# Kernel optimization log

Hardware: AMD Instinct MI355X
Metric: run time of the kernel (lower is better)

## Reference

```python
import jax, jax.numpy as jnp
import numpy as np

NUM_GRAPHS = 8
EV_A3_TO_GPA = 160.21766208


def _energy(pos, bond_vec, src, dst, edge_graph, centers, W1, b1, W2, b2, W3, b3):
    # Surrogate GNN energy: edge displacement mixes pos and bond_vec so both get grads,
    # mirroring grad(total_energies, [pos, bond_vec]) in the original wrapper.
    disp = bond_vec + pos[dst] - pos[src]                      # [E,3]
    d = jnp.sqrt(jnp.sum(disp * disp, axis=-1) + 1e-12)        # [E]
    rbf = jnp.exp(-jnp.square(d[:, None] - centers[None, :]))  # [E,K]
    h = jax.nn.silu(rbf @ W1 + b1)                             # [E,H]
    h = jax.nn.silu(h @ W2 + b2)                               # [E,H]
    e_edge = (h @ W3 + b3)[:, 0]                               # [E]
    return jax.ops.segment_sum(e_edge, edge_graph, num_segments=NUM_GRAPHS)  # [B]


def setup_inputs() -> dict:
    key = jax.random.key(0)
    ks = jax.random.split(key, 8)
    N, E, K, H = 49152, 786432, 32, 64
    pos = jax.random.normal(ks[0], (N, 3), jnp.float32) * 3.0
    bond_vec = jax.random.normal(ks[1], (E, 3), jnp.float32)
    src = jax.random.randint(ks[2], (E,), 0, N, dtype=jnp.int32)
    dst = jax.random.randint(ks[3], (E,), 0, N, dtype=jnp.int32)
    edge_graph = jnp.repeat(jnp.arange(NUM_GRAPHS, dtype=jnp.int32), E // NUM_GRAPHS)
    volume = jax.random.uniform(ks[4], (N,), jnp.float32, 50.0, 150.0)
    centers = jnp.linspace(0.0, 5.0, K).astype(jnp.float32)
    W1 = jax.random.normal(ks[5], (K, H), jnp.float32) / np.float32(np.sqrt(K))
    b1 = jnp.zeros((H,), jnp.float32)
    W2 = jax.random.normal(ks[6], (H, H), jnp.float32) / np.float32(np.sqrt(H))
    b2 = jnp.zeros((H,), jnp.float32)
    W3 = jax.random.normal(ks[7], (H, 1), jnp.float32) / np.float32(np.sqrt(H))
    b3 = jnp.zeros((1,), jnp.float32)
    return {"pos": pos, "bond_vec": bond_vec, "src": src, "dst": dst,
            "edge_graph": edge_graph, "volume": volume, "centers": centers,
            "W1": W1, "b1": b1, "W2": W2, "b2": b2, "W3": W3, "b3": b3}


def reference(pos, bond_vec, src, dst, edge_graph, volume, centers, W1, b1, W2, b2, W3, b3):
    energies, vjp_fn = jax.vjp(
        lambda p, bv: _energy(p, bv, src, dst, edge_graph, centers, W1, b1, W2, b2, W3, b3),
        pos, bond_vec)
    # grad_outputs = ones_like(total_energies)
    gpos, gbv = vjp_fn(jnp.ones_like(energies))
    forces = -gpos                                             # [N,3]
    f_ij = -gbv                                                # [E,3]
    # Per-graph stress: bond_vec_g^T @ f_ij_g, vectorized as segment-summed outer products.
    outer = bond_vec[:, :, None] * f_ij[:, None, :]            # [E,3,3]
    S = jax.ops.segment_sum(outer, edge_graph, num_segments=NUM_GRAPHS)  # [B,3,3]
    nodes_per_graph = pos.shape[0] // NUM_GRAPHS
    vol0 = volume[jnp.arange(NUM_GRAPHS) * nodes_per_graph]    # volume at first node of each graph
    stresses = (-EV_A3_TO_GPA * S / vol0[:, None, None]).reshape(NUM_GRAPHS * 3, 3)
    hessian = jnp.zeros((1,), jnp.float32)                     # calc_hessian=False
    return energies, forces, stresses, hessian
```

## Files before the change

### kernel.cpp

```cpp
#include <hip/hip_runtime.h>
#include <math.h>

#define K_RBF 32
#define H_DIM 64
#define TBL 4096
#define D_MAX 16.0f
#define N_NODES 49152
#define N_EDGES 786432
#define N_GRAPHS 8
#define NODES_PER_GRAPH 6144
#define EV_A3_TO_GPA 160.21766208f
#define LOG2E 1.44269504088896f

#define OUT_FORCES 8
#define OUT_STRESS 147464
#define OUT_TAIL_N 81

#define CHUNK_NODES  192
#define CHUNK_FLOATS 576
#define N_CHUNKS     256
#define REC_CAP      7168

#define EDGE_BLOCKS   384
#define EDGE_THREADS  1024
#define EDGES_PER_GRAPH (N_EDGES / N_GRAPHS)
#define BLK_PER_GRAPH 48

#define OFF_TAB 0u
#define OFF_CNT 32768u
#define OFF_REC 33792u
#define WS_NEED (OFF_REC + (size_t)N_CHUNKS * REC_CAP * 16u)

__device__ __forceinline__ int chunk_of(int node) {
    return (int)((unsigned)((node >> 6) * 683) >> 11);
}

__global__ __launch_bounds__(256) void build_table(
    const float* __restrict__ centers,
    const float* __restrict__ W1, const float* __restrict__ b1,
    const float* __restrict__ W2, const float* __restrict__ b2,
    const float* __restrict__ W3, const float* __restrict__ b3,
    float2* __restrict__ tab, int* __restrict__ gcnt,
    float* __restrict__ out, int zero_out_tail)
{
    if (blockIdx.x == 0) {
        int t = threadIdx.x;
        gcnt[t] = 0;
        if (zero_out_tail) {
            if (t < N_GRAPHS) out[t] = 0.f;
            else if (t < OUT_TAIL_N) out[3 * N_NODES + t] = 0.f;
        }
    }

    __shared__ float W2s[H_DIM * 65];
    for (int idx = threadIdx.x; idx < H_DIM * H_DIM; idx += 256)
        W2s[(idx >> 6) * 65 + (idx & 63)] = W2[idx];
    __syncthreads();

    int lane = threadIdx.x & 63;
    int i    = blockIdx.x * 4 + (threadIdx.x >> 6);
    float d  = (float)i * (D_MAX / (float)TBL);

    float z1 = b1[lane], u = 0.f;
#pragma unroll
    for (int k = 0; k < K_RBF; ++k) {
        float tc = d - centers[k];
        float e  = exp2f(-tc * tc * LOG2E);
        float w  = W1[k * H_DIM + lane];
        z1 = fmaf(e, w, z1);
        u  = fmaf(-2.f * tc * e, w, u);
    }
    float s1  = 1.f / (1.f + exp2f(-z1 * LOG2E));
    float h1  = z1 * s1;
    float ds1 = s1 * fmaf(z1, 1.f - s1, 1.f);

    float z2 = b2[lane];
#pragma unroll
    for (int h = 0; h < H_DIM; ++h)
        z2 = fmaf(__shfl(h1, h, 64), W2s[h * 65 + lane], z2);

    float s2  = 1.f / (1.f + exp2f(-z2 * LOG2E));
    float w3  = W3[lane];
    float Fp  = z2 * s2 * w3;
    float dz2 = w3 * s2 * fmaf(z2, 1.f - s2, 1.f);

    float dh1 = 0.f;
#pragma unroll
    for (int j = 0; j < H_DIM; ++j)
        dh1 = fmaf(__shfl(dz2, j, 64), W2s[lane * 65 + j], dh1);

    float Gp = dh1 * ds1 * u;
#pragma unroll
    for (int m = 32; m > 0; m >>= 1) {
        Fp += __shfl_xor(Fp, m, 64);
        Gp += __shfl_xor(Gp, m, 64);
    }
    if (lane == 0) tab[i] = make_float2(Fp + b3[0], Gp);
}

__global__ __launch_bounds__(EDGE_THREADS) void edge_compute(
    const float* __restrict__ pos, const float* __restrict__ bond,
    const int* __restrict__ src, const int* __restrict__ dst,
    const float* __restrict__ volume, const float2* __restrict__ tab,
    float4* __restrict__ recs, int* __restrict__ gcnt,
    float* __restrict__ out)
{
    __shared__ int   cnt[N_CHUNKS];
    __shared__ int   basech[N_CHUNKS];
    __shared__ float red[16][10];

    const int t = threadIdx.x;
    if (t < N_CHUNKS) cnt[t] = 0;
    __syncthreads();

    const int g = blockIdx.x & 7;
    const int w = blockIdx.x >> 3;
    const int base_e = g * EDGES_PER_GRAPH + w * (EDGE_THREADS * 2);

    float vacc[10];
#pragma unroll
    for (int q = 0; q < 10; ++q) vacc[q] = 0.f;

    int   edi[2], esi[2], es0[2], es1[2];
    float egx[2], egy[2], egz[2];

#pragma unroll
    for (int i = 0; i < 2; ++i) {
        int e  = base_e + i * EDGE_THREADS + t;
        int si = src[e], di = dst[e];
        float bx = bond[3 * e + 0], by = bond[3 * e + 1], bz = bond[3 * e + 2];
        float dx = bx + pos[3 * di + 0] - pos[3 * si + 0];
        float dy = by + pos[3 * di + 1] - pos[3 * si + 1];
        float dz = bz + pos[3 * di + 2] - pos[3 * si + 2];
        float d  = sqrtf(fmaf(dx, dx, fmaf(dy, dy, fmaf(dz, dz, 1e-12f))));

        float tt  = fminf(d * ((float)TBL / D_MAX), (float)(TBL - 1));
        int   ix  = min((int)tt, TBL - 2);
        float fr  = tt - (float)ix;
        float2 ta = tab[ix], tb2 = tab[ix + 1];
        float F = fmaf(fr, tb2.x - ta.x, ta.x);
        float G = fmaf(fr, tb2.y - ta.y, ta.y);

        float scl = G / d;
        float gx = scl * dx, gy = scl * dy, gz = scl * dz;
        egx[i] = gx; egy[i] = gy; egz[i] = gz;
        edi[i] = di; esi[i] = si;
        es0[i] = atomicAdd(&cnt[chunk_of(di)], 1);
        es1[i] = atomicAdd(&cnt[chunk_of(si)], 1);

        vacc[0] += F;
        vacc[1] = fmaf(bx, gx, vacc[1]); vacc[2] = fmaf(bx, gy, vacc[2]);
        vacc[3] = fmaf(bx, gz, vacc[3]); vacc[4] = fmaf(by, gx, vacc[4]);
        vacc[5] = fmaf(by, gy, vacc[5]); vacc[6] = fmaf(by, gz, vacc[6]);
        vacc[7] = fmaf(bz, gx, vacc[7]); vacc[8] = fmaf(bz, gy, vacc[8]);
        vacc[9] = fmaf(bz, gz, vacc[9]);
    }
    __syncthreads();
    if (t < N_CHUNKS) basech[t] = atomicAdd(&gcnt[t], cnt[t]);
    __syncthreads();
#pragma unroll
    for (int i = 0; i < 2; ++i) {
        int c0 = chunk_of(edi[i]), c1 = chunk_of(esi[i]);
        int l0 = edi[i] - c0 * CHUNK_NODES;
        int l1 = esi[i] - c1 * CHUNK_NODES;
        int p0 = basech[c0] + es0[i];
        int p1 = basech[c1] + es1[i];
        if (p0 < REC_CAP)
            recs[(size_t)c0 * REC_CAP + p0] =
                make_float4(-egx[i], -egy[i], -egz[i], __int_as_float(l0));
        if (p1 < REC_CAP)
            recs[(size_t)c1 * REC_CAP + p1] =
                make_float4(egx[i], egy[i], egz[i], __int_as_float(l1));
    }

#pragma unroll
    for (int q = 0; q < 10; ++q) {
        float x = vacc[q];
#pragma unroll
        for (int m = 32; m > 0; m >>= 1) x += __shfl_xor(x, m, 64);
        vacc[q] = x;
    }
    int wave = t >> 6;
    if ((t & 63) == 0)
#pragma unroll
        for (int q = 0; q < 10; ++q) red[wave][q] = vacc[q];
    __syncthreads();
    if (t < 10) {
        float tot = 0.f;
#pragma unroll
        for (int k = 0; k < 16; ++k) tot += red[k][t];
        if (t == 0) atomicAdd(out + g, tot);
        else {
            float vol = volume[g * NODES_PER_GRAPH];
            atomicAdd(out + OUT_STRESS + g * 9 + (t - 1),
                      tot * (EV_A3_TO_GPA / vol));
        }
    }
}

__global__ __launch_bounds__(512) void scatter_direct(
    const float4* __restrict__ recs, const int* __restrict__ gcnt,
    float* __restrict__ out)
{
    __shared__ float acc[CHUNK_FLOATS];
    const int t = threadIdx.x;
    if (t < CHUNK_FLOATS) acc[t] = 0.f;
    if (t < CHUNK_FLOATS - 512) acc[512 + t] = 0.f;
    __syncthreads();

    const int c = blockIdx.x;
    int total = min(gcnt[c], REC_CAP);
    const float4* seg = recs + (size_t)c * REC_CAP;
    for (int r = t; r < total; r += 512) {
        float4 rec = seg[r];
        int li = 3 * __float_as_int(rec.w);
        atomicAdd(&acc[li + 0], rec.x);
        atomicAdd(&acc[li + 1], rec.y);
        atomicAdd(&acc[li + 2], rec.z);
    }
    __syncthreads();

    if (t < CHUNK_FLOATS / 4) {
        float4* dst4 = (float4*)(out + OUT_FORCES + c * CHUNK_FLOATS);
        dst4[t] = ((const float4*)acc)[t];
    }
}

__global__ __launch_bounds__(256) void edge_fallback(
    const float* __restrict__ pos, const float* __restrict__ bond,
    const int* __restrict__ src, const int* __restrict__ dst,
    const float* __restrict__ volume, const float2* __restrict__ tab,
    float* __restrict__ out)
{
    __shared__ float red[4][10];
    int lb = (blockIdx.x & 7) * (EDGES_PER_GRAPH / 256) + (blockIdx.x >> 3);
    int g  = blockIdx.x & 7;
    int e  = lb * 256 + threadIdx.x;

    int si = src[e], di = dst[e];
    float bx = bond[3 * e + 0], by = bond[3 * e + 1], bz = bond[3 * e + 2];
    float dx = bx + pos[3 * di + 0] - pos[3 * si + 0];
    float dy = by + pos[3 * di + 1] - pos[3 * si + 1];
    float dz = bz + pos[3 * di + 2] - pos[3 * si + 2];
    float d  = sqrtf(fmaf(dx, dx, fmaf(dy, dy, fmaf(dz, dz, 1e-12f))));

    float tt  = fminf(d * ((float)TBL / D_MAX), (float)(TBL - 1));
    int   ix  = min((int)tt, TBL - 2);
    float fr  = tt - (float)ix;
    float2 ta = tab[ix], tb2 = tab[ix + 1];
    float F = fmaf(fr, tb2.x - ta.x, ta.x);
    float G = fmaf(fr, tb2.y - ta.y, ta.y);
    float scl = G / d;
    float gx = scl * dx, gy = scl * dy, gz = scl * dz;

    float* forces = out + OUT_FORCES;
    atomicAdd(forces + 3 * di + 0, -gx);
    atomicAdd(forces + 3 * di + 1, -gy);
    atomicAdd(forces + 3 * di + 2, -gz);
    atomicAdd(forces + 3 * si + 0,  gx);
    atomicAdd(forces + 3 * si + 1,  gy);
    atomicAdd(forces + 3 * si + 2,  gz);

    float v[10] = { F,
                    bx * gx, bx * gy, bx * gz,
                    by * gx, by * gy, by * gz,
                    bz * gx, bz * gy, bz * gz };
#pragma unroll
    for (int q = 0; q < 10; ++q) {
        float x = v[q];
#pragma unroll
        for (int m = 32; m > 0; m >>= 1) x += __shfl_xor(x, m, 64);
        v[q] = x;
    }
    int wave = threadIdx.x >> 6;
    if ((threadIdx.x & 63) == 0)
#pragma unroll
        for (int q = 0; q < 10; ++q) red[wave][q] = v[q];
    __syncthreads();
    if (threadIdx.x < 10) {
        float tot = red[0][threadIdx.x] + red[1][threadIdx.x]
                  + red[2][threadIdx.x] + red[3][threadIdx.x];
        if (threadIdx.x == 0) atomicAdd(out + g, tot);
        else {
            float vol = volume[g * NODES_PER_GRAPH];
            atomicAdd(out + OUT_STRESS + g * 9 + (threadIdx.x - 1),
                      tot * (EV_A3_TO_GPA / vol));
        }
    }
}

extern "C" void kernel_launch(void* const* d_in, const int* in_sizes, int n_in,
                              void* d_out, int out_size, void* d_ws, size_t ws_size,
                              hipStream_t stream)
{
    const float* pos     = (const float*)d_in[0];
    const float* bond    = (const float*)d_in[1];
    const int*   src     = (const int*)d_in[2];
    const int*   dst     = (const int*)d_in[3];
    const float* volume  = (const float*)d_in[5];
    const float* centers = (const float*)d_in[6];
    const float* W1 = (const float*)d_in[7];
    const float* b1 = (const float*)d_in[8];
    const float* W2 = (const float*)d_in[9];
    const float* b2 = (const float*)d_in[10];
    const float* W3 = (const float*)d_in[11];
    const float* b3 = (const float*)d_in[12];
    float*  out  = (float*)d_out;
    char*   ws   = (char*)d_ws;
    float2* tab  = (float2*)(ws + OFF_TAB);
    int*    gcnt = (int*)(ws + OFF_CNT);
    float4* recs = (float4*)(ws + OFF_REC);

    if (ws_size >= WS_NEED) {
        build_table<<<TBL / 4, 256, 0, stream>>>(centers, W1, b1, W2, b2, W3, b3,
                                                 tab, gcnt, out, 1);
        edge_compute<<<EDGE_BLOCKS, EDGE_THREADS, 0, stream>>>(
            pos, bond, src, dst, volume, tab, recs, gcnt, out);
        scatter_direct<<<N_CHUNKS, 512, 0, stream>>>(recs, gcnt, out);
    } else {
        hipMemsetAsync(d_out, 0, (size_t)out_size * sizeof(float), stream);
        build_table<<<TBL / 4, 256, 0, stream>>>(centers, W1, b1, W2, b2, W3, b3,
                                                 tab, gcnt, out, 0);
        edge_fallback<<<N_EDGES / 256, 256, 0, stream>>>(
            pos, bond, src, dst, volume, tab, out);
    }
}
```

Measured before the change: 150.7 us.

## Fuse table build, edge compute and scatter into one persistent kernel

After: 196.5 us. +30.4%, slower.

```diff
diff --git a/kernel.cpp b/kernel.cpp
--- a/kernel.cpp
+++ b/kernel.cpp
@@ -21,46 +21,30 @@
 #define N_CHUNKS     256
 #define REC_CAP      7168
 
-#define EDGE_BLOCKS   384
-#define EDGE_THREADS  1024
+#define FUSED_BLOCKS  256
+#define FUSED_THREADS 1024
+#define EDGES_PER_BLOCK 3072
 #define EDGES_PER_GRAPH (N_EDGES / N_GRAPHS)
-#define BLK_PER_GRAPH 48
-
-#define OFF_TAB 0u
-#define OFF_CNT 32768u
-#define OFF_REC 33792u
+#define BLK_PER_GRAPH 32
+#define TBL_PER_BLOCK 16
+
+#define OFF_TAB  0u
+#define OFF_CNT  32768u
+#define OFF_DONE 33792u
+#define OFF_REC  34816u
 #define WS_NEED (OFF_REC + (size_t)N_CHUNKS * REC_CAP * 16u)
 
 __device__ __forceinline__ int chunk_of(int node) {
     return (int)((unsigned)((node >> 6) * 683) >> 11);
 }
 
-__global__ __launch_bounds__(256) void build_table(
-    const float* __restrict__ centers,
+__device__ __forceinline__ float2 mlp_entry(
+    int i, int lane, const float* __restrict__ centers,
     const float* __restrict__ W1, const float* __restrict__ b1,
-    const float* __restrict__ W2, const float* __restrict__ b2,
-    const float* __restrict__ W3, const float* __restrict__ b3,
-    float2* __restrict__ tab, int* __restrict__ gcnt,
-    float* __restrict__ out, int zero_out_tail)
-{
-    if (blockIdx.x == 0) {
-        int t = threadIdx.x;
-        gcnt[t] = 0;
-        if (zero_out_tail) {
-            if (t < N_GRAPHS) out[t] = 0.f;
-            else if (t < OUT_TAIL_N) out[3 * N_NODES + t] = 0.f;
-        }
-    }
-
-    __shared__ float W2s[H_DIM * 65];
-    for (int idx = threadIdx.x; idx < H_DIM * H_DIM; idx += 256)
-        W2s[(idx >> 6) * 65 + (idx & 63)] = W2[idx];
-    __syncthreads();
-
-    int lane = threadIdx.x & 63;
-    int i    = blockIdx.x * 4 + (threadIdx.x >> 6);
+    const float* __restrict__ W2s, const float* __restrict__ b2,
+    const float* __restrict__ W3, const float* __restrict__ b3)
+{
     float d  = (float)i * (D_MAX / (float)TBL);
-
     float z1 = b1[lane], u = 0.f;
 #pragma unroll
     for (int k = 0; k < K_RBF; ++k) {
@@ -95,38 +79,72 @@
         Fp += __shfl_xor(Fp, m, 64);
         Gp += __shfl_xor(Gp, m, 64);
     }
-    if (lane == 0) tab[i] = make_float2(Fp + b3[0], Gp);
-}
-
-__global__ __launch_bounds__(EDGE_THREADS) void edge_compute(
+    return make_float2(Fp + b3[0], Gp);
+}
+
+__global__ __launch_bounds__(FUSED_THREADS, 4) void fused_all(
     const float* __restrict__ pos, const float* __restrict__ bond,
     const int* __restrict__ src, const int* __restrict__ dst,
-    const float* __restrict__ volume, const float2* __restrict__ tab,
-    float4* __restrict__ recs, int* __restrict__ gcnt,
-    float* __restrict__ out)
-{
-    __shared__ int   cnt[N_CHUNKS];
+    const float* __restrict__ volume, const float* __restrict__ centers,
+    const float* __restrict__ W1, const float* __restrict__ b1,
+    const float* __restrict__ W2, const float* __restrict__ b2,
+    const float* __restrict__ W3, const float* __restrict__ b3,
+    float2* __restrict__ tab, int* __restrict__ gcnt, int* __restrict__ done,
+    float4* __restrict__ recs, float* __restrict__ out)
+{
+    __shared__ float W2s[H_DIM * 65];
+    __shared__ int   cntl[N_CHUNKS];
     __shared__ int   basech[N_CHUNKS];
     __shared__ float red[16][10];
+    __shared__ float acc[4 * 577];
 
     const int t = threadIdx.x;
-    if (t < N_CHUNKS) cnt[t] = 0;
-    __syncthreads();
-
-    const int g = blockIdx.x & 7;
-    const int w = blockIdx.x >> 3;
-    const int base_e = g * EDGES_PER_GRAPH + w * (EDGE_THREADS * 2);
+    const int b = blockIdx.x;
+    const int lane = t & 63, wv = t >> 6;
+
+    for (int idx = t; idx < H_DIM * H_DIM; idx += FUSED_THREADS)
+        W2s[(idx >> 6) * 65 + (idx & 63)] = W2[idx];
+    if (b == 0) {
+        if (t < N_CHUNKS) gcnt[t] = 0;
+        if (t == 512) done[1] = 0;
+        if (t < N_GRAPHS) out[t] = 0.f;
+        else if (t >= 8 && t < OUT_TAIL_N) out[OUT_STRESS + t - 8] = 0.f;
+    }
+    __syncthreads();
+
+    {
+        int i = b * TBL_PER_BLOCK + wv;
+        float2 fg = mlp_entry(i, lane, centers, W1, b1, W2s, b2, W3, b3);
+        if (lane == 0) tab[i] = fg;
+    }
+    __syncthreads();
+
+    if (t == 0) {
+        __hip_atomic_fetch_add(&done[0], 1, __ATOMIC_RELEASE,
+                               __HIP_MEMORY_SCOPE_AGENT);
+        while (__hip_atomic_load(&done[0], __ATOMIC_ACQUIRE,
+                                 __HIP_MEMORY_SCOPE_AGENT) < FUSED_BLOCKS)
+            __builtin_amdgcn_s_sleep(2);
+    }
+    __syncthreads();
+
+    if (t < N_CHUNKS) cntl[t] = 0;
+    __syncthreads();
+
+    const int g = b >> 5;
+    const int w = b & 31;
+    const int base_e = g * EDGES_PER_GRAPH + w * EDGES_PER_BLOCK;
 
     float vacc[10];
 #pragma unroll
     for (int q = 0; q < 10; ++q) vacc[q] = 0.f;
 
-    int   edi[2], esi[2], es0[2], es1[2];
-    float egx[2], egy[2], egz[2];
-
-#pragma unroll
-    for (int i = 0; i < 2; ++i) {
-        int e  = base_e + i * EDGE_THREADS + t;
+    int   edi[3], esi[3], es0[3], es1[3];
+    float egx[3], egy[3], egz[3];
+
+#pragma unroll
+    for (int i = 0; i < 3; ++i) {
+        int e  = base_e + i * FUSED_THREADS + t;
         int si = src[e], di = dst[e];
         float bx = bond[3 * e + 0], by = bond[3 * e + 1], bz = bond[3 * e + 2];
         float dx = bx + pos[3 * di + 0] - pos[3 * si + 0];
@@ -145,8 +163,8 @@
         float gx = scl * dx, gy = scl * dy, gz = scl * dz;
         egx[i] = gx; egy[i] = gy; egz[i] = gz;
         edi[i] = di; esi[i] = si;
-        es0[i] = atomicAdd(&cnt[chunk_of(di)], 1);
-        es1[i] = atomicAdd(&cnt[chunk_of(si)], 1);
+        es0[i] = atomicAdd(&cntl[chunk_of(di)], 1);
+        es1[i] = atomicAdd(&cntl[chunk_of(si)], 1);
 
         vacc[0] += F;
         vacc[1] = fmaf(bx, gx, vacc[1]); vacc[2] = fmaf(bx, gy, vacc[2]);
@@ -156,10 +174,11 @@
         vacc[9] = fmaf(bz, gz, vacc[9]);
     }
     __syncthreads();
-    if (t < N_CHUNKS) basech[t] = atomicAdd(&gcnt[t], cnt[t]);
-    __syncthreads();
-#pragma unroll
-    for (int i = 0; i < 2; ++i) {
+    if (t < N_CHUNKS) basech[t] = atomicAdd(&gcnt[t], cntl[t]);
+    __syncthreads();
+
+#pragma unroll
+    for (int i = 0; i < 3; ++i) {
         int c0 = chunk_of(edi[i]), c1 = chunk_of(esi[i]);
         int l0 = edi[i] - c0 * CHUNK_NODES;
         int l1 = esi[i] - c1 * CHUNK_NODES;
@@ -180,10 +199,9 @@
         for (int m = 32; m > 0; m >>= 1) x += __shfl_xor(x, m, 64);
         vacc[q] = x;
     }
-    int wave = t >> 6;
-    if ((t & 63) == 0)
-#pragma unroll
-        for (int q = 0; q < 10; ++q) red[wave][q] = vacc[q];
+    if (lane == 0)
+#pragma unroll
+        for (int q = 0; q < 10; ++q) red[wv][q] = vacc[q];
     __syncthreads();
     if (t < 10) {
         float tot = 0.f;
@@ -196,34 +214,56 @@
                       tot * (EV_A3_TO_GPA / vol));
         }
     }
-}
-
-__global__ __launch_bounds__(512) void scatter_direct(
-    const float4* __restrict__ recs, const int* __restrict__ gcnt,
-    float* __restrict__ out)
-{
-    __shared__ float acc[CHUNK_FLOATS];
-    const int t = threadIdx.x;
-    if (t < CHUNK_FLOATS) acc[t] = 0.f;
-    if (t < CHUNK_FLOATS - 512) acc[512 + t] = 0.f;
-    __syncthreads();
-
-    const int c = blockIdx.x;
-    int total = min(gcnt[c], REC_CAP);
-    const float4* seg = recs + (size_t)c * REC_CAP;
-    for (int r = t; r < total; r += 512) {
-        float4 rec = seg[r];
-        int li = 3 * __float_as_int(rec.w);
-        atomicAdd(&acc[li + 0], rec.x);
-        atomicAdd(&acc[li + 1], rec.y);
-        atomicAdd(&acc[li + 2], rec.z);
-    }
-    __syncthreads();
-
-    if (t < CHUNK_FLOATS / 4) {
-        float4* dst4 = (float4*)(out + OUT_FORCES + c * CHUNK_FLOATS);
-        dst4[t] = ((const float4*)acc)[t];
-    }
+    __syncthreads();
+
+    if (t == 0) {
+        __hip_atomic_fetch_add(&done[1], 1, __ATOMIC_RELEASE,
+                               __HIP_MEMORY_SCOPE_AGENT);
+        while (__hip_atomic_load(&done[1], __ATOMIC_ACQUIRE,
+                                 __HIP_MEMORY_SCOPE_AGENT) < FUSED_BLOCKS)
+            __builtin_amdgcn_s_sleep(2);
+    }
+    __syncthreads();
+
+    for (int j = t; j < 4 * 577; j += FUSED_THREADS) acc[j] = 0.f;
+    __syncthreads();
+
+    {
+        const int c = b;
+        int total = min(gcnt[c], REC_CAP);
+        const float4* seg = recs + (size_t)c * REC_CAP;
+        const int rep = (t & 3) * 577;
+        for (int r = t; r < total; r += FUSED_THREADS) {
+            float4 rec = seg[r];
+            int li = 3 * __float_as_int(rec.w);
+            atomicAdd(&acc[rep + li + 0], rec.x);
+            atomicAdd(&acc[rep + li + 1], rec.y);
+            atomicAdd(&acc[rep + li + 2], rec.z);
+        }
+        __syncthreads();
+        if (t < CHUNK_FLOATS) {
+            float s = acc[t] + acc[577 + t] + acc[2 * 577 + t] + acc[3 * 577 + t];
+            out[OUT_FORCES + c * CHUNK_FLOATS + t] = s;
+        }
+    }
+}
+
+__global__ __launch_bounds__(256) void build_table(
+    const float* __restrict__ centers,
+    const float* __restrict__ W1, const float* __restrict__ b1,
+    const float* __restrict__ W2, const float* __restrict__ b2,
+    const float* __restrict__ W3, const float* __restrict__ b3,
+    float2* __restrict__ tab)
+{
+    __shared__ float W2s[H_DIM * 65];
+    for (int idx = threadIdx.x; idx < H_DIM * H_DIM; idx += 256)
+        W2s[(idx >> 6) * 65 + (idx & 63)] = W2[idx];
+    __syncthreads();
+
+    int lane = threadIdx.x & 63;
+    int i    = blockIdx.x * 4 + (threadIdx.x >> 6);
+    float2 fg = mlp_entry(i, lane, centers, W1, b1, W2s, b2, W3, b3);
+    if (lane == 0) tab[i] = fg;
 }
 
 __global__ __launch_bounds__(256) void edge_fallback(
@@ -309,18 +349,17 @@
     char*   ws   = (char*)d_ws;
     float2* tab  = (float2*)(ws + OFF_TAB);
     int*    gcnt = (int*)(ws + OFF_CNT);
+    int*    done = (int*)(ws + OFF_DONE);
     float4* recs = (float4*)(ws + OFF_REC);
 
     if (ws_size >= WS_NEED) {
-        build_table<<<TBL / 4, 256, 0, stream>>>(centers, W1, b1, W2, b2, W3, b3,
-                                                 tab, gcnt, out, 1);
-        edge_compute<<<EDGE_BLOCKS, EDGE_THREADS, 0, stream>>>(
-            pos, bond, src, dst, volume, tab, recs, gcnt, out);
-        scatter_direct<<<N_CHUNKS, 512, 0, stream>>>(recs, gcnt, out);
+        hipMemsetAsync(done, 0, 4, stream);
+        fused_all<<<FUSED_BLOCKS, FUSED_THREADS, 0, stream>>>(
+            pos, bond, src, dst, volume, centers,
+            W1, b1, W2, b2, W3, b3, tab, gcnt, done, recs, out);
     } else {
         hipMemsetAsync(d_out, 0, (size_t)out_size * sizeof(float), stream);
-        build_table<<<TBL / 4, 256, 0, stream>>>(centers, W1, b1, W2, b2, W3, b3,
-                                                 tab, gcnt, out, 0);
+        build_table<<<TBL / 4, 256, 0, stream>>>(centers, W1, b1, W2, b2, W3, b3, tab);
         edge_fallback<<<N_EDGES / 256, 256, 0, stream>>>(
             pos, bond, src, dst, volume, tab, out);
     }
```

## Replace global bucket atomics with fixed per-block record slots

Applied to the files above, without the earlier changes.

New measurement: 159.6 us. +5.9%, slower.

```diff
diff --git a/kernel.cpp b/kernel.cpp
--- a/kernel.cpp
+++ b/kernel.cpp
@@ -19,48 +19,31 @@
 #define CHUNK_NODES  192
 #define CHUNK_FLOATS 576
 #define N_CHUNKS     256
-#define REC_CAP      7168
-
-#define EDGE_BLOCKS   384
-#define EDGE_THREADS  1024
+
+#define EDGE_BLOCKS   1536
+#define EDGE_THREADS  512
 #define EDGES_PER_GRAPH (N_EDGES / N_GRAPHS)
-#define BLK_PER_GRAPH 48
+#define BLK_PER_GRAPH 192
+
+#define SLOT_CAP   32
+#define CAP_SHIFT  5
 
 #define OFF_TAB 0u
 #define OFF_CNT 32768u
-#define OFF_REC 33792u
-#define WS_NEED (OFF_REC + (size_t)N_CHUNKS * REC_CAP * 16u)
+#define OFF_REC (32768u + (unsigned)(N_CHUNKS * EDGE_BLOCKS * 4))
+#define WS_NEED ((size_t)OFF_REC + (size_t)N_CHUNKS * EDGE_BLOCKS * SLOT_CAP * 16u)
 
 __device__ __forceinline__ int chunk_of(int node) {
     return (int)((unsigned)((node >> 6) * 683) >> 11);
 }
 
-__global__ __launch_bounds__(256) void build_table(
-    const float* __restrict__ centers,
+__device__ __forceinline__ float2 mlp_entry(
+    int i, int lane, const float* __restrict__ centers,
     const float* __restrict__ W1, const float* __restrict__ b1,
-    const float* __restrict__ W2, const float* __restrict__ b2,
-    const float* __restrict__ W3, const float* __restrict__ b3,
-    float2* __restrict__ tab, int* __restrict__ gcnt,
-    float* __restrict__ out, int zero_out_tail)
-{
-    if (blockIdx.x == 0) {
-        int t = threadIdx.x;
-        gcnt[t] = 0;
-        if (zero_out_tail) {
-            if (t < N_GRAPHS) out[t] = 0.f;
-            else if (t < OUT_TAIL_N) out[3 * N_NODES + t] = 0.f;
-        }
-    }
-
-    __shared__ float W2s[H_DIM * 65];
-    for (int idx = threadIdx.x; idx < H_DIM * H_DIM; idx += 256)
-        W2s[(idx >> 6) * 65 + (idx & 63)] = W2[idx];
-    __syncthreads();
-
-    int lane = threadIdx.x & 63;
-    int i    = blockIdx.x * 4 + (threadIdx.x >> 6);
+    const float* __restrict__ W2s, const float* __restrict__ b2,
+    const float* __restrict__ W3, const float* __restrict__ b3)
+{
     float d  = (float)i * (D_MAX / (float)TBL);
-
     float z1 = b1[lane], u = 0.f;
 #pragma unroll
     for (int k = 0; k < K_RBF; ++k) {
@@ -95,84 +78,82 @@
         Fp += __shfl_xor(Fp, m, 64);
         Gp += __shfl_xor(Gp, m, 64);
     }
-    if (lane == 0) tab[i] = make_float2(Fp + b3[0], Gp);
+    return make_float2(Fp + b3[0], Gp);
+}
+
+__global__ __launch_bounds__(256) void build_table(
+    const float* __restrict__ centers,
+    const float* __restrict__ W1, const float* __restrict__ b1,
+    const float* __restrict__ W2, const float* __restrict__ b2,
+    const float* __restrict__ W3, const float* __restrict__ b3,
+    float2* __restrict__ tab, float* __restrict__ out, int zero_out_tail)
+{
+    if (blockIdx.x == 0 && zero_out_tail) {
+        int t = threadIdx.x;
+        if (t < N_GRAPHS) out[t] = 0.f;
+        else if (t < OUT_TAIL_N) out[3 * N_NODES + t] = 0.f;
+    }
+
+    __shared__ float W2s[H_DIM * 65];
+    for (int idx = threadIdx.x; idx < H_DIM * H_DIM; idx += 256)
+        W2s[(idx >> 6) * 65 + (idx & 63)] = W2[idx];
+    __syncthreads();
+
+    int lane = threadIdx.x & 63;
+    int i    = blockIdx.x * 4 + (threadIdx.x >> 6);
+    float2 fg = mlp_entry(i, lane, centers, W1, b1, W2s, b2, W3, b3);
+    if (lane == 0) tab[i] = fg;
 }
 
 __global__ __launch_bounds__(EDGE_THREADS) void edge_compute(
     const float* __restrict__ pos, const float* __restrict__ bond,
     const int* __restrict__ src, const int* __restrict__ dst,
     const float* __restrict__ volume, const float2* __restrict__ tab,
-    float4* __restrict__ recs, int* __restrict__ gcnt,
+    float4* __restrict__ recs, int* __restrict__ cnttab,
     float* __restrict__ out)
 {
     __shared__ int   cnt[N_CHUNKS];
-    __shared__ int   basech[N_CHUNKS];
-    __shared__ float red[16][10];
+    __shared__ float red[8][10];
 
     const int t = threadIdx.x;
+    const int b = blockIdx.x;
     if (t < N_CHUNKS) cnt[t] = 0;
     __syncthreads();
 
-    const int g = blockIdx.x & 7;
-    const int w = blockIdx.x >> 3;
-    const int base_e = g * EDGES_PER_GRAPH + w * (EDGE_THREADS * 2);
-
-    float vacc[10];
-#pragma unroll
-    for (int q = 0; q < 10; ++q) vacc[q] = 0.f;
-
-    int   edi[2], esi[2], es0[2], es1[2];
-    float egx[2], egy[2], egz[2];
-
-#pragma unroll
-    for (int i = 0; i < 2; ++i) {
-        int e  = base_e + i * EDGE_THREADS + t;
-        int si = src[e], di = dst[e];
-        float bx = bond[3 * e + 0], by = bond[3 * e + 1], bz = bond[3 * e + 2];
-        float dx = bx + pos[3 * di + 0] - pos[3 * si + 0];
-        float dy = by + pos[3 * di + 1] - pos[3 * si + 1];
-        float dz = bz + pos[3 * di + 2] - pos[3 * si + 2];
-        float d  = sqrtf(fmaf(dx, dx, fmaf(dy, dy, fmaf(dz, dz, 1e-12f))));
-
-        float tt  = fminf(d * ((float)TBL / D_MAX), (float)(TBL - 1));
-        int   ix  = min((int)tt, TBL - 2);
-        float fr  = tt - (float)ix;
-        float2 ta = tab[ix], tb2 = tab[ix + 1];
-        float F = fmaf(fr, tb2.x - ta.x, ta.x);
-        float G = fmaf(fr, tb2.y - ta.y, ta.y);
-
-        float scl = G / d;
-        float gx = scl * dx, gy = scl * dy, gz = scl * dz;
-        egx[i] = gx; egy[i] = gy; egz[i] = gz;
-        edi[i] = di; esi[i] = si;
-        es0[i] = atomicAdd(&cnt[chunk_of(di)], 1);
-        es1[i] = atomicAdd(&cnt[chunk_of(si)], 1);
-
-        vacc[0] += F;
-        vacc[1] = fmaf(bx, gx, vacc[1]); vacc[2] = fmaf(bx, gy, vacc[2]);
-        vacc[3] = fmaf(bx, gz, vacc[3]); vacc[4] = fmaf(by, gx, vacc[4]);
-        vacc[5] = fmaf(by, gy, vacc[5]); vacc[6] = fmaf(by, gz, vacc[6]);
-        vacc[7] = fmaf(bz, gx, vacc[7]); vacc[8] = fmaf(bz, gy, vacc[8]);
-        vacc[9] = fmaf(bz, gz, vacc[9]);
-    }
-    __syncthreads();
-    if (t < N_CHUNKS) basech[t] = atomicAdd(&gcnt[t], cnt[t]);
-    __syncthreads();
-#pragma unroll
-    for (int i = 0; i < 2; ++i) {
-        int c0 = chunk_of(edi[i]), c1 = chunk_of(esi[i]);
-        int l0 = edi[i] - c0 * CHUNK_NODES;
-        int l1 = esi[i] - c1 * CHUNK_NODES;
-        int p0 = basech[c0] + es0[i];
-        int p1 = basech[c1] + es1[i];
-        if (p0 < REC_CAP)
-            recs[(size_t)c0 * REC_CAP + p0] =
-                make_float4(-egx[i], -egy[i], -egz[i], __int_as_float(l0));
-        if (p1 < REC_CAP)
-            recs[(size_t)c1 * REC_CAP + p1] =
-                make_float4(egx[i], egy[i], egz[i], __int_as_float(l1));
-    }
-
+    const int e = b * EDGE_THREADS + t;
+    const int g = b / BLK_PER_GRAPH;
+
+    int si = src[e], di = dst[e];
+    float bx = bond[3 * e + 0], by = bond[3 * e + 1], bz = bond[3 * e + 2];
+    float dx = bx + pos[3 * di + 0] - pos[3 * si + 0];
+    float dy = by + pos[3 * di + 1] - pos[3 * si + 1];
+    float dz = bz + pos[3 * di + 2] - pos[3 * si + 2];
+    float d  = sqrtf(fmaf(dx, dx, fmaf(dy, dy, fmaf(dz, dz, 1e-12f))));
+
+    float tt  = fminf(d * ((float)TBL / D_MAX), (float)(TBL - 1));
+    int   ix  = min((int)tt, TBL - 2);
+    float fr  = tt - (float)ix;
+    float2 ta = tab[ix], tb2 = tab[ix + 1];
+    float F = fmaf(fr, tb2.x - ta.x, ta.x);
+    float G = fmaf(fr, tb2.y - ta.y, ta.y);
+
+    float scl = G / d;
+    float gx = scl * dx, gy = scl * dy, gz = scl * dz;
+
+    int c0 = chunk_of(di), c1 = chunk_of(si);
+    int r0 = atomicAdd(&cnt[c0], 1);
+    int r1 = atomicAdd(&cnt[c1], 1);
+    if (r0 < SLOT_CAP)
+        recs[((size_t)c0 * EDGE_BLOCKS + b) * SLOT_CAP + r0] =
+            make_float4(-gx, -gy, -gz, __int_as_float(di - c0 * CHUNK_NODES));
+    if (r1 < SLOT_CAP)
+        recs[((size_t)c1 * EDGE_BLOCKS + b) * SLOT_CAP + r1] =
+            make_float4(gx, gy, gz, __int_as_float(si - c1 * CHUNK_NODES));
+
+    float vacc[10] = { F,
+                       bx * gx, bx * gy, bx * gz,
+                       by * gx, by * gy, by * gz,
+                       bz * gx, bz * gy, bz * gz };
 #pragma unroll
     for (int q = 0; q < 10; ++q) {
         float x = vacc[q];
@@ -185,10 +166,14 @@
 #pragma unroll
         for (int q = 0; q < 10; ++q) red[wave][q] = vacc[q];
     __syncthreads();
+
+    if (t < N_CHUNKS)
+        cnttab[(size_t)t * EDGE_BLOCKS + b] = min(cnt[t], SLOT_CAP);
+
     if (t < 10) {
         float tot = 0.f;
 #pragma unroll
-        for (int k = 0; k < 16; ++k) tot += red[k][t];
+        for (int k = 0; k < 8; ++k) tot += red[k][t];
         if (t == 0) atomicAdd(out + g, tot);
         else {
             float vol = volume[g * NODES_PER_GRAPH];
@@ -198,32 +183,36 @@
     }
 }
 
-__global__ __launch_bounds__(512) void scatter_direct(
-    const float4* __restrict__ recs, const int* __restrict__ gcnt,
+__global__ __launch_bounds__(1024) void scatter_direct(
+    const float4* __restrict__ recs, const int* __restrict__ cnttab,
     float* __restrict__ out)
 {
     __shared__ float acc[CHUNK_FLOATS];
+    __shared__ int   cl[EDGE_BLOCKS];
     const int t = threadIdx.x;
+    const int c = blockIdx.x;
     if (t < CHUNK_FLOATS) acc[t] = 0.f;
-    if (t < CHUNK_FLOATS - 512) acc[512 + t] = 0.f;
-    __syncthreads();
-
-    const int c = blockIdx.x;
-    int total = min(gcnt[c], REC_CAP);
-    const float4* seg = recs + (size_t)c * REC_CAP;
-    for (int r = t; r < total; r += 512) {
-        float4 rec = seg[r];
-        int li = 3 * __float_as_int(rec.w);
-        atomicAdd(&acc[li + 0], rec.x);
-        atomicAdd(&acc[li + 1], rec.y);
-        atomicAdd(&acc[li + 2], rec.z);
-    }
-    __syncthreads();
-
-    if (t < CHUNK_FLOATS / 4) {
-        float4* dst4 = (float4*)(out + OUT_FORCES + c * CHUNK_FLOATS);
-        dst4[t] = ((const float4*)acc)[t];
-    }
+    for (int j = t; j < EDGE_BLOCKS; j += 1024)
+        cl[j] = cnttab[(size_t)c * EDGE_BLOCKS + j];
+    __syncthreads();
+
+    const float4* seg = recs + (size_t)c * EDGE_BLOCKS * SLOT_CAP;
+#pragma unroll 4
+    for (int j = t; j < EDGE_BLOCKS * SLOT_CAP; j += 1024) {
+        int bb = j >> CAP_SHIFT;
+        int s  = j & (SLOT_CAP - 1);
+        if (s < cl[bb]) {
+            float4 rec = seg[j];
+            int li = 3 * __float_as_int(rec.w);
+            atomicAdd(&acc[li + 0], rec.x);
+            atomicAdd(&acc[li + 1], rec.y);
+            atomicAdd(&acc[li + 2], rec.z);
+        }
+    }
+    __syncthreads();
+
+    if (t < CHUNK_FLOATS)
+        out[OUT_FORCES + c * CHUNK_FLOATS + t] = acc[t];
 }
 
 __global__ __launch_bounds__(256) void edge_fallback(
@@ -305,22 +294,22 @@
     const float* b2 = (const float*)d_in[10];
     const float* W3 = (const float*)d_in[11];
     const float* b3 = (const float*)d_in[12];
-    float*  out  = (float*)d_out;
-    char*   ws   = (char*)d_ws;
-    float2* tab  = (float2*)(ws + OFF_TAB);
-    int*    gcnt = (int*)(ws + OFF_CNT);
-    float4* recs = (float4*)(ws + OFF_REC);
+    float*  out    = (float*)d_out;
+    char*   ws     = (char*)d_ws;
+    float2* tab    = (float2*)(ws + OFF_TAB);
+    int*    cnttab = (int*)(ws + OFF_CNT);
+    float4* recs   = (float4*)(ws + OFF_REC);
 
     if (ws_size >= WS_NEED) {
         build_table<<<TBL / 4, 256, 0, stream>>>(centers, W1, b1, W2, b2, W3, b3,
-                                                 tab, gcnt, out, 1);
+                                                 tab, out, 1);
         edge_compute<<<EDGE_BLOCKS, EDGE_THREADS, 0, stream>>>(
-            pos, bond, src, dst, volume, tab, recs, gcnt, out);
-        scatter_direct<<<N_CHUNKS, 512, 0, stream>>>(recs, gcnt, out);
+            pos, bond, src, dst, volume, tab, recs, cnttab, out);
+        scatter_direct<<<N_CHUNKS, 1024, 0, stream>>>(recs, cnttab, out);
     } else {
         hipMemsetAsync(d_out, 0, (size_t)out_size * sizeof(float), stream);
         build_table<<<TBL / 4, 256, 0, stream>>>(centers, W1, b1, W2, b2, W3, b3,
-                                                 tab, gcnt, out, 0);
+                                                 tab, out, 0);
         edge_fallback<<<N_EDGES / 256, 256, 0, stream>>>(
             pos, bond, src, dst, volume, tab, out);
     }
```
